# Optimization experiments

Measured on AMD Instinct MI355X. Metric: run time of the kernel, lower is better.

The kernel has to match this reference:

```python
import jax, jax.numpy as jnp
import numpy as np

N_NODES = 100000
N_EDGES = 1600000
IN_C, HID_C, OUT_C = 128, 128, 64


def gcn_conv(x, src, dst, n_nodes, W, b):
    # PyG GCNConv (normalize=True, add_self_loops=True):
    # out = D^{-1/2} (A+I) D^{-1/2} (x @ W^T) + b
    h = x @ W.T                                   # [N, out]
    deg = jax.ops.segment_sum(jnp.ones(src.shape, x.dtype), dst,
                              num_segments=n_nodes)  # includes self-loops
    dinv = jnp.where(deg > 0, jax.lax.rsqrt(deg), 0.0)
    norm = dinv[src] * dinv[dst]                  # [E+N]
    msg = h[src] * norm[:, None]                  # gather + scale
    out = jax.ops.segment_sum(msg, dst, num_segments=n_nodes)
    return out + b


def setup_inputs() -> dict:
    key = jax.random.key(0)
    ks = jax.random.split(key, 8)
    x = jax.random.normal(ks[0], (N_NODES, IN_C), dtype=jnp.float32)
    edge_index = jax.random.randint(ks[1], (2, N_EDGES), 0, N_NODES, dtype=jnp.int64)

    def lin(k, fan_out, fan_in):
        s = 1.0 / np.sqrt(fan_in)
        kw, kb = jax.random.split(k)
        W = jax.random.uniform(kw, (fan_out, fan_in), jnp.float32, -s, s)
        b = jax.random.uniform(kb, (fan_out,), jnp.float32, -s, s)
        return W, b

    W1, b1 = lin(ks[2], HID_C, IN_C)
    W2, b2 = lin(ks[3], HID_C, HID_C)
    W3, b3 = lin(ks[4], OUT_C, HID_C)
    return {"x": x, "edge_index": edge_index,
            "W1": W1, "b1": b1, "W2": W2, "b2": b2, "W3": W3, "b3": b3}


def reference(x, edge_index, W1, b1, W2, b2, W3, b3):
    n = x.shape[0]
    loop = jnp.arange(n, dtype=edge_index.dtype)
    src = jnp.concatenate([edge_index[0], loop])  # add self-loops once; identical per layer
    dst = jnp.concatenate([edge_index[1], loop])
    h = gcn_conv(x, src, dst, n, W1, b1)
    h = jax.nn.relu(h)
    h = gcn_conv(h, src, dst, n, W2, b2)
    h = jax.nn.relu(h)
    h = gcn_conv(h, src, dst, n, W3, b3)
    return h
```

## Files before the change

kernel.cpp:

```cpp
#include <hip/hip_runtime.h>


#define NPB 256
#define CAP 4672
#define BIN_WGS 512

typedef short bfrag __attribute__((ext_vector_type(8)));
typedef float f32x4 __attribute__((ext_vector_type(4)));
typedef unsigned short u16x8 __attribute__((ext_vector_type(8)));

__global__ __launch_bounds__(256) void bin_edges(const int* __restrict__ src,
                                                 const int* __restrict__ dst,
                                                 int* __restrict__ cur,
                                                 int* __restrict__ binned,
                                                 int E, int B) {
  __shared__ int lc[512];
  __shared__ int lbase[512];
  const int t = threadIdx.x;
  const int chunk = (E + BIN_WGS - 1) / BIN_WGS;
  const int e0 = blockIdx.x * chunk;
  const int e1 = min(E, e0 + chunk);

  for (int i = t; i < B; i += 256) lc[i] = 0;
  __syncthreads();
  for (int e = e0 + t; e < e1; e += 256) {
    int d = dst[e];
    atomicAdd(&lc[d >> 8], 1);
  }
  __syncthreads();
  for (int i = t; i < B; i += 256) {
    int c = lc[i];
    lbase[i] = c ? atomicAdd(&cur[i], c) : 0;
    lc[i] = 0;
  }
  __syncthreads();
  for (int e = e0 + t; e < e1; e += 256) {
    int d = dst[e];
    int s = __builtin_nontemporal_load(&src[e]);
    int bk = d >> 8;
    int p = lbase[bk] + atomicAdd(&lc[bk], 1);
    if (p < (bk + 1) * CAP)
      binned[p] = ((d & 255) << 24) | s;
  }
}

__global__ __launch_bounds__(256) void build_buckets(const int* __restrict__ binned,
                                                     const int* __restrict__ cur,
                                                     int* __restrict__ cols,
                                                     int2* __restrict__ off2,
                                                     float* __restrict__ dinv,
                                                     int N) {
  __shared__ int eb[CAP];
  __shared__ int ob[CAP];
  __shared__ int lc[256];
  __shared__ int sc[256];
  const int b = blockIdx.x;
  const int t = threadIdx.x;
  const int base = b * CAP;
  const int cntb = min(cur[b] - base, CAP);

  for (int i = t; i < cntb; i += 256) eb[i] = binned[base + i];
  lc[t] = 0;
  __syncthreads();
  for (int i = t; i < cntb; i += 256)
    atomicAdd(&lc[(unsigned)eb[i] >> 24], 1);
  __syncthreads();
  int myc = lc[t];
  sc[t] = myc;
  __syncthreads();
  for (int d = 1; d < 256; d <<= 1) {
    int a = (t >= d) ? sc[t - d] : 0;
    __syncthreads();
    sc[t] += a;
    __syncthreads();
  }
  int excl = sc[t] - myc;
  int node = b * NPB + t;
  if (node < N) {
    off2[node] = make_int2(base + excl, base + excl + myc);
    dinv[node] = rsqrtf((float)(myc + 1));
  }
  lc[t] = excl;
  __syncthreads();
  for (int i = t; i < cntb; i += 256) {
    int e = eb[i];
    int p = atomicAdd(&lc[(unsigned)e >> 24], 1);
    ob[p] = e & 0xFFFFFF;
  }
  __syncthreads();
  for (int i = t; i < cntb; i += 256) cols[base + i] = ob[i];
}

__device__ inline unsigned short bf16rne(float x) {
  unsigned u = __float_as_uint(x);
  return (unsigned short)((u + 0x7FFFu + ((u >> 16) & 1u)) >> 16);
}
__device__ inline float bf16lo(unsigned q) { return __uint_as_float(q << 16); }
__device__ inline float bf16hi(unsigned q) { return __uint_as_float(q & 0xFFFF0000u); }

__global__ __launch_bounds__(256) void split_w3(const float* __restrict__ W1,
                                                const float* __restrict__ W2,
                                                const float* __restrict__ W3,
                                                unsigned short* __restrict__ w1h,
                                                unsigned short* __restrict__ w1l,
                                                unsigned short* __restrict__ w2h,
                                                unsigned short* __restrict__ w2l,
                                                unsigned short* __restrict__ w3h,
                                                unsigned short* __restrict__ w3l,
                                                int* __restrict__ cur, int B) {
  int i = blockIdx.x * 256 + threadIdx.x;
  const float* W;
  unsigned short *hi, *lo;
  int j;
  if (i < 16384) {
    W = W1; hi = w1h; lo = w1l; j = i;
  } else if (i < 32768) {
    W = W2; hi = w2h; lo = w2l; j = i - 16384;
  } else if (i < 40960) {
    W = W3; hi = w3h; lo = w3l; j = i - 32768;
  } else if (i < 40960 + B) {
    cur[i - 40960] = (i - 40960) * CAP;
    return;
  } else {
    return;
  }
  float v = W[j];
  unsigned short h = bf16rne(v);
  hi[j] = h;
  lo[j] = bf16rne(v - __uint_as_float((unsigned)h << 16));
}

#define LDP 136

template <int OUTC, bool CSOUT>
__global__ __launch_bounds__(256) void gemm_planes_p(const unsigned short* __restrict__ Xh,
                                                     const unsigned short* __restrict__ Xl,
                                                     const unsigned short* __restrict__ Whg,
                                                     const unsigned short* __restrict__ Wlg,
                                                     const float* __restrict__ dinv,
                                                     unsigned short* __restrict__ Y,
                                                     int M, int ntiles) {
  constexpr int CT = OUTC / 16;
  __shared__ unsigned short Whi[OUTC * LDP], Wlo[OUTC * LDP];
  const int tid = threadIdx.x;

  for (int idx = tid; idx < OUTC * 16; idx += 256) {
    int r = idx >> 4, g = idx & 15;
    *(u16x8*)(Whi + r * LDP + g * 8) = *(const u16x8*)(Whg + (size_t)r * 128 + g * 8);
    *(u16x8*)(Wlo + r * LDP + g * 8) = *(const u16x8*)(Wlg + (size_t)r * 128 + g * 8);
  }
  __syncthreads();

  const int lane = tid & 63;
  const int wv = tid >> 6;
  const int col_l = lane & 15;
  const int quad = lane >> 4;
  const int bBase = col_l * LDP + quad * 8;
  const int G = gridDim.x;

  int tt = blockIdx.x;
  if (tt >= ntiles) return;

  bfrag aH[4], aL[4], nH[4], nL[4];
  {
    const size_t arow = (size_t)min(tt * 64 + wv * 16 + col_l, M - 1) * 128;
#pragma unroll
    for (int ks = 0; ks < 4; ++ks) {
      aH[ks] = *(const bfrag*)(Xh + arow + ks * 32 + quad * 8);
      aL[ks] = *(const bfrag*)(Xl + arow + ks * 32 + quad * 8);
    }
  }

  while (true) {
    const int tn = tt + G;
    const bool have_next = tn < ntiles;
    if (have_next) {
      const size_t arow = (size_t)min(tn * 64 + wv * 16 + col_l, M - 1) * 128;
#pragma unroll
      for (int ks = 0; ks < 4; ++ks) {
        nH[ks] = *(const bfrag*)(Xh + arow + ks * 32 + quad * 8);
        nL[ks] = *(const bfrag*)(Xl + arow + ks * 32 + quad * 8);
      }
    }

    f32x4 acc[CT];
#pragma unroll
    for (int ct = 0; ct < CT; ++ct) acc[ct] = {0.f, 0.f, 0.f, 0.f};
#pragma unroll
    for (int ks = 0; ks < 4; ++ks) {
#pragma unroll
      for (int ct = 0; ct < CT; ++ct) {
        int bo = bBase + ct * 16 * LDP + ks * 32;
        bfrag bHi = *(const bfrag*)(Whi + bo);
        bfrag bLo = *(const bfrag*)(Wlo + bo);
        acc[ct] = __builtin_amdgcn_mfma_f32_16x16x32_bf16(aH[ks], bHi, acc[ct], 0, 0, 0);
        acc[ct] = __builtin_amdgcn_mfma_f32_16x16x32_bf16(aL[ks], bHi, acc[ct], 0, 0, 0);
        acc[ct] = __builtin_amdgcn_mfma_f32_16x16x32_bf16(aH[ks], bLo, acc[ct], 0, 0, 0);
      }
    }

#pragma unroll
    for (int r = 0; r < 4; ++r) {
      int row = tt * 64 + wv * 16 + quad * 4 + r;
      if (row < M) {
        float s = dinv[row];
#pragma unroll
        for (int ct = 0; ct < CT; ++ct) {
          unsigned short h = bf16rne(acc[ct][r] * s);
          if (CSOUT)
            Y[((size_t)(ct >> 2) * M + row) * 64 + (ct & 3) * 16 + col_l] = h;
          else
            Y[(size_t)row * OUTC + ct * 16 + col_l] = h;
        }
      }
    }

    if (!have_next) break;
#pragma unroll
    for (int ks = 0; ks < 4; ++ks) { aH[ks] = nH[ks]; aL[ks] = nL[ks]; }
    tt = tn;
  }
}

template <int OUTC, bool CSOUT>
__global__ __launch_bounds__(256) void gemm_xsplit_p(const float* __restrict__ X,
                                                     const unsigned short* __restrict__ Whg,
                                                     const unsigned short* __restrict__ Wlg,
                                                     const float* __restrict__ dinv,
                                                     unsigned short* __restrict__ Y,
                                                     int M, int ntiles) {
  constexpr int CT = OUTC / 16;
  __shared__ unsigned short Whi[OUTC * LDP], Wlo[OUTC * LDP];
  const int tid = threadIdx.x;

  for (int idx = tid; idx < OUTC * 16; idx += 256) {
    int r = idx >> 4, g = idx & 15;
    *(u16x8*)(Whi + r * LDP + g * 8) = *(const u16x8*)(Whg + (size_t)r * 128 + g * 8);
    *(u16x8*)(Wlo + r * LDP + g * 8) = *(const u16x8*)(Wlg + (size_t)r * 128 + g * 8);
  }
  __syncthreads();

  const int lane = tid & 63;
  const int wv = tid >> 6;
  const int col_l = lane & 15;
  const int quad = lane >> 4;
  const int bBase = col_l * LDP + quad * 8;
  const int G = gridDim.x;

  int tt = blockIdx.x;
  if (tt >= ntiles) return;

  float4 r0[4], r1[4], n0[4], n1[4];
  {
    const size_t arow = (size_t)min(tt * 64 + wv * 16 + col_l, M - 1) * 128;
#pragma unroll
    for (int ks = 0; ks < 4; ++ks) {
      r0[ks] = *(const float4*)(X + arow + ks * 32 + quad * 8);
      r1[ks] = *(const float4*)(X + arow + ks * 32 + quad * 8 + 4);
    }
  }

  while (true) {
    const int tn = tt + G;
    const bool have_next = tn < ntiles;
    if (have_next) {
      const size_t arow = (size_t)min(tn * 64 + wv * 16 + col_l, M - 1) * 128;
#pragma unroll
      for (int ks = 0; ks < 4; ++ks) {
        n0[ks] = *(const float4*)(X + arow + ks * 32 + quad * 8);
        n1[ks] = *(const float4*)(X + arow + ks * 32 + quad * 8 + 4);
      }
    }

    bfrag aH[4], aL[4];
#pragma unroll
    for (int ks = 0; ks < 4; ++ks) {
      float vv[8] = {r0[ks].x, r0[ks].y, r0[ks].z, r0[ks].w,
                     r1[ks].x, r1[ks].y, r1[ks].z, r1[ks].w};
#pragma unroll
      for (int j = 0; j < 8; ++j) {
        unsigned short h = bf16rne(vv[j]);
        aH[ks][j] = (short)h;
        aL[ks][j] = (short)bf16rne(vv[j] - __uint_as_float((unsigned)h << 16));
      }
    }

    f32x4 acc[CT];
#pragma unroll
    for (int ct = 0; ct < CT; ++ct) acc[ct] = {0.f, 0.f, 0.f, 0.f};
#pragma unroll
    for (int ks = 0; ks < 4; ++ks) {
#pragma unroll
      for (int ct = 0; ct < CT; ++ct) {
        int bo = bBase + ct * 16 * LDP + ks * 32;
        bfrag bHi = *(const bfrag*)(Whi + bo);
        bfrag bLo = *(const bfrag*)(Wlo + bo);
        acc[ct] = __builtin_amdgcn_mfma_f32_16x16x32_bf16(aH[ks], bHi, acc[ct], 0, 0, 0);
        acc[ct] = __builtin_amdgcn_mfma_f32_16x16x32_bf16(aL[ks], bHi, acc[ct], 0, 0, 0);
        acc[ct] = __builtin_amdgcn_mfma_f32_16x16x32_bf16(aH[ks], bLo, acc[ct], 0, 0, 0);
      }
    }

#pragma unroll
    for (int r = 0; r < 4; ++r) {
      int row = tt * 64 + wv * 16 + quad * 4 + r;
      if (row < M) {
        float s = dinv[row];
#pragma unroll
        for (int ct = 0; ct < CT; ++ct) {
          unsigned short h = bf16rne(acc[ct][r] * s);
          if (CSOUT)
            Y[((size_t)(ct >> 2) * M + row) * 64 + (ct & 3) * 16 + col_l] = h;
          else
            Y[(size_t)row * OUTC + ct * 16 + col_l] = h;
        }
      }
    }

    if (!have_next) break;
#pragma unroll
    for (int ks = 0; ks < 4; ++ks) { r0[ks] = n0[ks]; r1[ks] = n1[ks]; }
    tt = tn;
  }
}

__device__ inline void acc_add(float* a, uint4 d) {
  a[0] += bf16lo(d.x); a[1] += bf16hi(d.x);
  a[2] += bf16lo(d.y); a[3] += bf16hi(d.y);
  a[4] += bf16lo(d.z); a[5] += bf16hi(d.z);
  a[6] += bf16lo(d.w); a[7] += bf16hi(d.w);
}

__global__ __launch_bounds__(256) void aggregate_h2(const unsigned short* __restrict__ xs,
                                                    const int2* __restrict__ off2,
                                                    const int* __restrict__ cols,
                                                    const float* __restrict__ dinv,
                                                    const float* __restrict__ bias,
                                                    unsigned short* __restrict__ oh,
                                                    unsigned short* __restrict__ ol,
                                                    int N) {
  const int cg = blockIdx.x & 1;
  const int tile = blockIdx.x >> 1;
  const int t = threadIdx.x;
  const int gl = t & 7;
  const int node = tile * 32 + (t >> 3);
  if (node >= N) return;

  const char* xb = (const char*)xs + (size_t)cg * N * 128;
  const unsigned go = (unsigned)gl * 16;

  float acc[8];
  {
    uint4 d = *(const uint4*)(xb + (size_t)node * 128 + go);
    acc[0] = bf16lo(d.x); acc[1] = bf16hi(d.x);
    acc[2] = bf16lo(d.y); acc[3] = bf16hi(d.y);
    acc[4] = bf16lo(d.z); acc[5] = bf16hi(d.z);
    acc[6] = bf16lo(d.w); acc[7] = bf16hi(d.w);
  }

  const int2 oo = off2[node];
  const int en = oo.y;
  for (int e0 = oo.x; e0 < en; e0 += 8) {
    int col = __builtin_nontemporal_load(&cols[min(e0 + gl, en - 1)]);
    int m = en - e0;
    if (m > 8) m = 8;
    const int c1 = m - 1;
    for (int j = 0; j < m; j += 4) {
      int s0 = __shfl(col, min(j,     c1), 8);
      int s1 = __shfl(col, min(j + 1, c1), 8);
      int s2 = __shfl(col, min(j + 2, c1), 8);
      int s3 = __shfl(col, min(j + 3, c1), 8);
      uint4 d0 = *(const uint4*)(xb + (size_t)s0 * 128 + go);
      uint4 d1 = *(const uint4*)(xb + (size_t)s1 * 128 + go);
      uint4 d2 = *(const uint4*)(xb + (size_t)s2 * 128 + go);
      uint4 d3 = *(const uint4*)(xb + (size_t)s3 * 128 + go);
      acc_add(acc, d0);
      if (j + 1 < m) acc_add(acc, d1);
      if (j + 2 < m) acc_add(acc, d2);
      if (j + 3 < m) acc_add(acc, d3);
    }
  }

  const float dd = dinv[node];
  const float4 bA = *(const float4*)(bias + cg * 64 + gl * 8);
  const float4 bB = *(const float4*)(bias + cg * 64 + gl * 8 + 4);
  float h[8];
  h[0] = acc[0] * dd + bA.x; h[1] = acc[1] * dd + bA.y;
  h[2] = acc[2] * dd + bA.z; h[3] = acc[3] * dd + bA.w;
  h[4] = acc[4] * dd + bB.x; h[5] = acc[5] * dd + bB.y;
  h[6] = acc[6] * dd + bB.z; h[7] = acc[7] * dd + bB.w;
#pragma unroll
  for (int q = 0; q < 8; ++q) h[q] = fmaxf(h[q], 0.f);

  u16x8 hv, lv;
#pragma unroll
  for (int q = 0; q < 8; ++q) {
    unsigned short hb = bf16rne(h[q]);
    hv[q] = hb;
    lv[q] = bf16rne(h[q] - __uint_as_float((unsigned)hb << 16));
  }
  const size_t ob = (size_t)node * 128 + cg * 64 + gl * 8;
  __builtin_nontemporal_store(hv, (u16x8*)(oh + ob));
  __builtin_nontemporal_store(lv, (u16x8*)(ol + ob));
}

template <int C, bool RELU, bool SPLIT>
__global__ __launch_bounds__(256) void aggregate4(const unsigned short* __restrict__ xs,
                                                  const int2* __restrict__ off2,
                                                  const int* __restrict__ cols,
                                                  const float* __restrict__ dinv,
                                                  const float* __restrict__ bias,
                                                  float* __restrict__ outf,
                                                  unsigned short* __restrict__ oh,
                                                  unsigned short* __restrict__ ol,
                                                  int N) {
  constexpr int GL = C / 8;
  constexpr int LSH = (GL == 16) ? 4 : 3;
  constexpr int NPBk = 256 / GL;
  const int t = threadIdx.x;
  const int gl = t & (GL - 1);
  const int node = blockIdx.x * NPBk + (t >> LSH);
  if (node >= N) return;

  const unsigned co = (unsigned)gl * 16;
  const char* xb = (const char*)xs;

  float acc[8];
  {
    uint4 d = *(const uint4*)(xb + (size_t)node * (C * 2) + co);
    acc[0] = bf16lo(d.x); acc[1] = bf16hi(d.x);
    acc[2] = bf16lo(d.y); acc[3] = bf16hi(d.y);
    acc[4] = bf16lo(d.z); acc[5] = bf16hi(d.z);
    acc[6] = bf16lo(d.w); acc[7] = bf16hi(d.w);
  }

  const int2 oo = off2[node];
  const int en = oo.y;
  for (int e0 = oo.x; e0 < en; e0 += GL) {
    int col = __builtin_nontemporal_load(&cols[min(e0 + gl, en - 1)]);
    int m = en - e0;
    if (m > GL) m = GL;
    const int c1 = m - 1;
    for (int j = 0; j < m; j += 4) {
      int s0 = __shfl(col, min(j,     c1), GL);
      int s1 = __shfl(col, min(j + 1, c1), GL);
      int s2 = __shfl(col, min(j + 2, c1), GL);
      int s3 = __shfl(col, min(j + 3, c1), GL);
      uint4 d0 = *(const uint4*)(xb + (size_t)s0 * (C * 2) + co);
      uint4 d1 = *(const uint4*)(xb + (size_t)s1 * (C * 2) + co);
      uint4 d2 = *(const uint4*)(xb + (size_t)s2 * (C * 2) + co);
      uint4 d3 = *(const uint4*)(xb + (size_t)s3 * (C * 2) + co);
      acc_add(acc, d0);
      if (j + 1 < m) acc_add(acc, d1);
      if (j + 2 < m) acc_add(acc, d2);
      if (j + 3 < m) acc_add(acc, d3);
    }
  }

  const float dd = dinv[node];
  const float4 bA = *(const float4*)(bias + gl * 8);
  const float4 bB = *(const float4*)(bias + gl * 8 + 4);
  float h[8];
  h[0] = acc[0] * dd + bA.x; h[1] = acc[1] * dd + bA.y;
  h[2] = acc[2] * dd + bA.z; h[3] = acc[3] * dd + bA.w;
  h[4] = acc[4] * dd + bB.x; h[5] = acc[5] * dd + bB.y;
  h[6] = acc[6] * dd + bB.z; h[7] = acc[7] * dd + bB.w;
  if (RELU) {
#pragma unroll
    for (int q = 0; q < 8; ++q) h[q] = fmaxf(h[q], 0.f);
  }
  if (SPLIT) {
    u16x8 hv, lv;
#pragma unroll
    for (int q = 0; q < 8; ++q) {
      unsigned short hb = bf16rne(h[q]);
      hv[q] = hb;
      lv[q] = bf16rne(h[q] - __uint_as_float((unsigned)hb << 16));
    }
    __builtin_nontemporal_store(hv, (u16x8*)(oh + (size_t)node * C + gl * 8));
    __builtin_nontemporal_store(lv, (u16x8*)(ol + (size_t)node * C + gl * 8));
  } else {
    f32x4 oA = {h[0], h[1], h[2], h[3]};
    f32x4 oB = {h[4], h[5], h[6], h[7]};
    __builtin_nontemporal_store(oA, (f32x4*)(outf + (size_t)node * C + gl * 8));
    __builtin_nontemporal_store(oB, (f32x4*)(outf + (size_t)node * C + gl * 8 + 4));
  }
}


extern "C" void kernel_launch(void* const* d_in, const int* in_sizes, int n_in,
                              void* d_out, int out_size, void* d_ws, size_t ws_size,
                              hipStream_t stream) {
  const float* x  = (const float*)d_in[0];
  const int*   ei = (const int*)d_in[1];
  const float* W1 = (const float*)d_in[2];
  const float* b1 = (const float*)d_in[3];
  const float* W2 = (const float*)d_in[4];
  const float* b2 = (const float*)d_in[5];
  const float* W3 = (const float*)d_in[6];
  const float* b3 = (const float*)d_in[7];

  const int N = in_sizes[0] / 128;
  const int E = in_sizes[1] / 2;
  const int* src = ei;
  const int* dst = ei + E;
  const int B = (N + NPB - 1) / NPB;

  char* w = (char*)d_ws;
  size_t p = 0;
  auto alloc = [&](size_t bytes) -> void* {
    void* r = w + p;
    p = (p + bytes + 255) & ~(size_t)255;
    return r;
  };
  float*    dinv   = (float*)alloc((size_t)N * 4);
  int2*     off2   = (int2*)alloc((size_t)N * 8);
  int*      cur    = (int*)alloc((size_t)B * 4);
  int*      binned = (int*)alloc((size_t)B * CAP * 4);
  int*      cols   = (int*)alloc((size_t)B * CAP * 4);
  unsigned short* xsb = (unsigned short*)alloc((size_t)N * 128 * 2);
  unsigned short* hh  = (unsigned short*)alloc((size_t)N * 128 * 2);
  unsigned short* hl  = (unsigned short*)alloc((size_t)N * 128 * 2);
  unsigned short* w1h = (unsigned short*)alloc(128 * 128 * 2);
  unsigned short* w1l = (unsigned short*)alloc(128 * 128 * 2);
  unsigned short* w2h = (unsigned short*)alloc(128 * 128 * 2);
  unsigned short* w2l = (unsigned short*)alloc(128 * 128 * 2);
  unsigned short* w3h = (unsigned short*)alloc(64 * 128 * 2);
  unsigned short* w3l = (unsigned short*)alloc(64 * 128 * 2);

  split_w3<<<(40960 + B + 255) / 256, 256, 0, stream>>>(W1, W2, W3, w1h, w1l,
                                                        w2h, w2l, w3h, w3l,
                                                        cur, B);
  bin_edges<<<BIN_WGS, 256, 0, stream>>>(src, dst, cur, binned, E, B);
  build_buckets<<<B, 256, 0, stream>>>(binned, cur, cols, off2, dinv, N);

  const int ntiles = (N + 63) / 64;
  const int G128 = 512;
  const int G64  = 1024;
  const int T = (N + 31) / 32;
  const int ab64 = (N + 31) / 32;

  gemm_xsplit_p<128, true><<<G128, 256, 0, stream>>>(x, w1h, w1l, dinv, xsb, N, ntiles);
  aggregate_h2<<<T * 2, 256, 0, stream>>>(xsb, off2, cols, dinv, b1, hh, hl, N);
  gemm_planes_p<128, true><<<G128, 256, 0, stream>>>(hh, hl, w2h, w2l, dinv, xsb, N, ntiles);
  aggregate_h2<<<T * 2, 256, 0, stream>>>(xsb, off2, cols, dinv, b2, hh, hl, N);
  gemm_planes_p<64, false><<<G64, 256, 0, stream>>>(hh, hl, w3h, w3l, dinv, xsb, N, ntiles);
  aggregate4<64, false, false><<<ab64, 256, 0, stream>>>(xsb, off2, cols, dinv, b3,
                                                         (float*)d_out, nullptr,
                                                         nullptr, N);
}
```

Before: 382.9 us.

## Keep GEMM weight fragments in registers and split output columns across waves

The GEMM kernels no longer stage the split weight planes in LDS. Each wave now loads its own 64-column slice of the hi/lo weight fragments into registers once, and waves are split between row groups and column halves, so each block handles 32 rows for 128-wide outputs. This removes per-tile LDS reads of B and the initial LDS fill and barrier. The cost is much higher register pressure (32 bfrag weights per lane, with launch_bounds(256,2)), more tiles per kernel for the 128-wide layers, and reloading the activation rows once per column-half wave.

```diff
diff --git a/kernel.cpp b/kernel.cpp
--- a/kernel.cpp
+++ b/kernel.cpp
@@ -130,40 +130,45 @@
   lo[j] = bf16rne(v - __uint_as_float((unsigned)h << 16));
 }
 
-#define LDP 136
 
 template <int OUTC, bool CSOUT>
-__global__ __launch_bounds__(256) void gemm_planes_p(const unsigned short* __restrict__ Xh,
-                                                     const unsigned short* __restrict__ Xl,
-                                                     const unsigned short* __restrict__ Whg,
-                                                     const unsigned short* __restrict__ Wlg,
-                                                     const float* __restrict__ dinv,
-                                                     unsigned short* __restrict__ Y,
-                                                     int M, int ntiles) {
-  constexpr int CT = OUTC / 16;
-  __shared__ unsigned short Whi[OUTC * LDP], Wlo[OUTC * LDP];
+__global__ __launch_bounds__(256, 2) void gemm_planes_r(const unsigned short* __restrict__ Xh,
+                                                        const unsigned short* __restrict__ Xl,
+                                                        const unsigned short* __restrict__ Whg,
+                                                        const unsigned short* __restrict__ Wlg,
+                                                        const float* __restrict__ dinv,
+                                                        unsigned short* __restrict__ Y,
+                                                        int M, int ntiles) {
+  constexpr int WC = OUTC / 64;
+  constexpr int TROWS = 64 / WC;
   const int tid = threadIdx.x;
-
-  for (int idx = tid; idx < OUTC * 16; idx += 256) {
-    int r = idx >> 4, g = idx & 15;
-    *(u16x8*)(Whi + r * LDP + g * 8) = *(const u16x8*)(Whg + (size_t)r * 128 + g * 8);
-    *(u16x8*)(Wlo + r * LDP + g * 8) = *(const u16x8*)(Wlg + (size_t)r * 128 + g * 8);
-  }
-  __syncthreads();
-
   const int lane = tid & 63;
   const int wv = tid >> 6;
+  const int wm = wv / WC;
+  const int wc = wv % WC;
   const int col_l = lane & 15;
   const int quad = lane >> 4;
-  const int bBase = col_l * LDP + quad * 8;
   const int G = gridDim.x;
+
+  bfrag wH[4][4], wL[4][4];
+  {
+    const unsigned short* wb = Whg + (size_t)(wc * 64 + col_l) * 128 + quad * 8;
+    const unsigned short* wl = Wlg + (size_t)(wc * 64 + col_l) * 128 + quad * 8;
+#pragma unroll
+    for (int ct = 0; ct < 4; ++ct)
+#pragma unroll
+      for (int ks = 0; ks < 4; ++ks) {
+        wH[ks][ct] = *(const bfrag*)(wb + ct * 16 * 128 + ks * 32);
+        wL[ks][ct] = *(const bfrag*)(wl + ct * 16 * 128 + ks * 32);
+      }
+  }
 
   int tt = blockIdx.x;
   if (tt >= ntiles) return;
 
   bfrag aH[4], aL[4], nH[4], nL[4];
   {
-    const size_t arow = (size_t)min(tt * 64 + wv * 16 + col_l, M - 1) * 128;
+    const size_t arow = (size_t)min(tt * TROWS + wm * 16 + col_l, M - 1) * 128;
 #pragma unroll
     for (int ks = 0; ks < 4; ++ks) {
       aH[ks] = *(const bfrag*)(Xh + arow + ks * 32 + quad * 8);
@@ -175,7 +180,7 @@
     const int tn = tt + G;
     const bool have_next = tn < ntiles;
     if (have_next) {
-      const size_t arow = (size_t)min(tn * 64 + wv * 16 + col_l, M - 1) * 128;
+      const size_t arow = (size_t)min(tn * TROWS + wm * 16 + col_l, M - 1) * 128;
 #pragma unroll
       for (int ks = 0; ks < 4; ++ks) {
         nH[ks] = *(const bfrag*)(Xh + arow + ks * 32 + quad * 8);
@@ -183,34 +188,31 @@
       }
     }
 
-    f32x4 acc[CT];
-#pragma unroll
-    for (int ct = 0; ct < CT; ++ct) acc[ct] = {0.f, 0.f, 0.f, 0.f};
+    f32x4 acc[4];
+#pragma unroll
+    for (int ct = 0; ct < 4; ++ct) acc[ct] = {0.f, 0.f, 0.f, 0.f};
 #pragma unroll
     for (int ks = 0; ks < 4; ++ks) {
 #pragma unroll
-      for (int ct = 0; ct < CT; ++ct) {
-        int bo = bBase + ct * 16 * LDP + ks * 32;
-        bfrag bHi = *(const bfrag*)(Whi + bo);
-        bfrag bLo = *(const bfrag*)(Wlo + bo);
-        acc[ct] = __builtin_amdgcn_mfma_f32_16x16x32_bf16(aH[ks], bHi, acc[ct], 0, 0, 0);
-        acc[ct] = __builtin_amdgcn_mfma_f32_16x16x32_bf16(aL[ks], bHi, acc[ct], 0, 0, 0);
-        acc[ct] = __builtin_amdgcn_mfma_f32_16x16x32_bf16(aH[ks], bLo, acc[ct], 0, 0, 0);
+      for (int ct = 0; ct < 4; ++ct) {
+        acc[ct] = __builtin_amdgcn_mfma_f32_16x16x32_bf16(aH[ks], wH[ks][ct], acc[ct], 0, 0, 0);
+        acc[ct] = __builtin_amdgcn_mfma_f32_16x16x32_bf16(aL[ks], wH[ks][ct], acc[ct], 0, 0, 0);
+        acc[ct] = __builtin_amdgcn_mfma_f32_16x16x32_bf16(aH[ks], wL[ks][ct], acc[ct], 0, 0, 0);
       }
     }
 
 #pragma unroll
     for (int r = 0; r < 4; ++r) {
-      int row = tt * 64 + wv * 16 + quad * 4 + r;
+      int row = tt * TROWS + wm * 16 + quad * 4 + r;
       if (row < M) {
         float s = dinv[row];
 #pragma unroll
-        for (int ct = 0; ct < CT; ++ct) {
+        for (int ct = 0; ct < 4; ++ct) {
           unsigned short h = bf16rne(acc[ct][r] * s);
           if (CSOUT)
-            Y[((size_t)(ct >> 2) * M + row) * 64 + (ct & 3) * 16 + col_l] = h;
+            Y[((size_t)wc * M + row) * 64 + ct * 16 + col_l] = h;
           else
-            Y[(size_t)row * OUTC + ct * 16 + col_l] = h;
+            Y[(size_t)row * OUTC + wc * 64 + ct * 16 + col_l] = h;
         }
       }
     }
@@ -223,36 +225,42 @@
 }
 
 template <int OUTC, bool CSOUT>
-__global__ __launch_bounds__(256) void gemm_xsplit_p(const float* __restrict__ X,
-                                                     const unsigned short* __restrict__ Whg,
-                                                     const unsigned short* __restrict__ Wlg,
-                                                     const float* __restrict__ dinv,
-                                                     unsigned short* __restrict__ Y,
-                                                     int M, int ntiles) {
-  constexpr int CT = OUTC / 16;
-  __shared__ unsigned short Whi[OUTC * LDP], Wlo[OUTC * LDP];
+__global__ __launch_bounds__(256, 2) void gemm_xsplit_r(const float* __restrict__ X,
+                                                        const unsigned short* __restrict__ Whg,
+                                                        const unsigned short* __restrict__ Wlg,
+                                                        const float* __restrict__ dinv,
+                                                        unsigned short* __restrict__ Y,
+                                                        int M, int ntiles) {
+  constexpr int WC = OUTC / 64;
+  constexpr int TROWS = 64 / WC;
   const int tid = threadIdx.x;
-
-  for (int idx = tid; idx < OUTC * 16; idx += 256) {
-    int r = idx >> 4, g = idx & 15;
-    *(u16x8*)(Whi + r * LDP + g * 8) = *(const u16x8*)(Whg + (size_t)r * 128 + g * 8);
-    *(u16x8*)(Wlo + r * LDP + g * 8) = *(const u16x8*)(Wlg + (size_t)r * 128 + g * 8);
-  }
-  __syncthreads();
-
   const int lane = tid & 63;
   const int wv = tid >> 6;
+  const int wm = wv / WC;
+  const int wc = wv % WC;
   const int col_l = lane & 15;
   const int quad = lane >> 4;
-  const int bBase = col_l * LDP + quad * 8;
   const int G = gridDim.x;
+
+  bfrag wH[4][4], wL[4][4];
+  {
+    const unsigned short* wb = Whg + (size_t)(wc * 64 + col_l) * 128 + quad * 8;
+    const unsigned short* wl = Wlg + (size_t)(wc * 64 + col_l) * 128 + quad * 8;
+#pragma unroll
+    for (int ct = 0; ct < 4; ++ct)
+#pragma unroll
+      for (int ks = 0; ks < 4; ++ks) {
+        wH[ks][ct] = *(const bfrag*)(wb + ct * 16 * 128 + ks * 32);
+        wL[ks][ct] = *(const bfrag*)(wl + ct * 16 * 128 + ks * 32);
+      }
+  }
 
   int tt = blockIdx.x;
   if (tt >= ntiles) return;
 
   float4 r0[4], r1[4], n0[4], n1[4];
   {
-    const size_t arow = (size_t)min(tt * 64 + wv * 16 + col_l, M - 1) * 128;
+    const size_t arow = (size_t)min(tt * TROWS + wm * 16 + col_l, M - 1) * 128;
 #pragma unroll
     for (int ks = 0; ks < 4; ++ks) {
       r0[ks] = *(const float4*)(X + arow + ks * 32 + quad * 8);
@@ -264,7 +272,7 @@
     const int tn = tt + G;
     const bool have_next = tn < ntiles;
     if (have_next) {
-      const size_t arow = (size_t)min(tn * 64 + wv * 16 + col_l, M - 1) * 128;
+      const size_t arow = (size_t)min(tn * TROWS + wm * 16 + col_l, M - 1) * 128;
 #pragma unroll
       for (int ks = 0; ks < 4; ++ks) {
         n0[ks] = *(const float4*)(X + arow + ks * 32 + quad * 8);
@@ -285,34 +293,31 @@
       }
     }
 
-    f32x4 acc[CT];
-#pragma unroll
-    for (int ct = 0; ct < CT; ++ct) acc[ct] = {0.f, 0.f, 0.f, 0.f};
+    f32x4 acc[4];
+#pragma unroll
+    for (int ct = 0; ct < 4; ++ct) acc[ct] = {0.f, 0.f, 0.f, 0.f};
 #pragma unroll
     for (int ks = 0; ks < 4; ++ks) {
 #pragma unroll
-      for (int ct = 0; ct < CT; ++ct) {
-        int bo = bBase + ct * 16 * LDP + ks * 32;
-        bfrag bHi = *(const bfrag*)(Whi + bo);
-        bfrag bLo = *(const bfrag*)(Wlo + bo);
-        acc[ct] = __builtin_amdgcn_mfma_f32_16x16x32_bf16(aH[ks], bHi, acc[ct], 0, 0, 0);
-        acc[ct] = __builtin_amdgcn_mfma_f32_16x16x32_bf16(aL[ks], bHi, acc[ct], 0, 0, 0);
-        acc[ct] = __builtin_amdgcn_mfma_f32_16x16x32_bf16(aH[ks], bLo, acc[ct], 0, 0, 0);
+      for (int ct = 0; ct < 4; ++ct) {
+        acc[ct] = __builtin_amdgcn_mfma_f32_16x16x32_bf16(aH[ks], wH[ks][ct], acc[ct], 0, 0, 0);
+        acc[ct] = __builtin_amdgcn_mfma_f32_16x16x32_bf16(aL[ks], wH[ks][ct], acc[ct], 0, 0, 0);
+        acc[ct] = __builtin_amdgcn_mfma_f32_16x16x32_bf16(aH[ks], wL[ks][ct], acc[ct], 0, 0, 0);
       }
     }
 
 #pragma unroll
     for (int r = 0; r < 4; ++r) {
-      int row = tt * 64 + wv * 16 + quad * 4 + r;
+      int row = tt * TROWS + wm * 16 + quad * 4 + r;
       if (row < M) {
         float s = dinv[row];
 #pragma unroll
-        for (int ct = 0; ct < CT; ++ct) {
+        for (int ct = 0; ct < 4; ++ct) {
           unsigned short h = bf16rne(acc[ct][r] * s);
           if (CSOUT)
-            Y[((size_t)(ct >> 2) * M + row) * 64 + (ct & 3) * 16 + col_l] = h;
+            Y[((size_t)wc * M + row) * 64 + ct * 16 + col_l] = h;
           else
-            Y[(size_t)row * OUTC + ct * 16 + col_l] = h;
+            Y[(size_t)row * OUTC + wc * 64 + ct * 16 + col_l] = h;
         }
       }
     }
@@ -534,17 +539,17 @@
   bin_edges<<<BIN_WGS, 256, 0, stream>>>(src, dst, cur, binned, E, B);
   build_buckets<<<B, 256, 0, stream>>>(binned, cur, cols, off2, dinv, N);
 
-  const int ntiles = (N + 63) / 64;
-  const int G128 = 512;
-  const int G64  = 1024;
+  const int nt32 = (N + 31) / 32;
+  const int nt64 = (N + 63) / 64;
+  const int G = 512;
   const int T = (N + 31) / 32;
   const int ab64 = (N + 31) / 32;
 
-  gemm_xsplit_p<128, true><<<G128, 256, 0, stream>>>(x, w1h, w1l, dinv, xsb, N, ntiles);
+  gemm_xsplit_r<128, true><<<G, 256, 0, stream>>>(x, w1h, w1l, dinv, xsb, N, nt32);
   aggregate_h2<<<T * 2, 256, 0, stream>>>(xsb, off2, cols, dinv, b1, hh, hl, N);
-  gemm_planes_p<128, true><<<G128, 256, 0, stream>>>(hh, hl, w2h, w2l, dinv, xsb, N, ntiles);
+  gemm_planes_r<128, true><<<G, 256, 0, stream>>>(hh, hl, w2h, w2l, dinv, xsb, N, nt32);
   aggregate_h2<<<T * 2, 256, 0, stream>>>(xsb, off2, cols, dinv, b2, hh, hl, N);
-  gemm_planes_p<64, false><<<G64, 256, 0, stream>>>(hh, hl, w3h, w3l, dinv, xsb, N, ntiles);
+  gemm_planes_r<64, false><<<G, 256, 0, stream>>>(hh, hl, w3h, w3l, dinv, xsb, N, nt64);
   aggregate4<64, false, false><<<ab64, 256, 0, stream>>>(xsb, off2, cols, dinv, b3,
                                                          (float*)d_out, nullptr,
                                                          nullptr, N);
```

After: 391.2 us. 1.02x slower.
